# Performance work log

Hardware: AMD Instinct MI355X
Metric: run time of the kernel (lower is better)

The kernel has to match this reference:

```python
import jax, jax.numpy as jnp
import numpy as np

L, M, B = 32768, 8, 8192      # lines, max neighbors per line, blocks
LIN, BIN, H = 768, 768, 512   # line_in_dim, block_in_dim, hidden_size
NH, DH = 8, 512 // 8          # heads, head_dim
LN_EPS = 1e-5


def _ln(x, g, b):
    mu = jnp.mean(x, axis=-1, keepdims=True)
    var = jnp.mean(jnp.square(x - mu), axis=-1, keepdims=True)
    return (x - mu) * jax.lax.rsqrt(var + LN_EPS) * g + b


def setup_inputs() -> dict:
    key = jax.random.key(0)
    ks = jax.random.split(key, 12)
    w = lambda k, shape, fan: jax.random.normal(k, shape, jnp.float32) * (fan ** -0.5)
    return {
        'global_lines': jax.random.normal(ks[0], (L, LIN), jnp.float32),
        'block_reprs': jax.random.normal(ks[1], (B, BIN), jnp.float32),
        'Wq': w(ks[2], (H, LIN), LIN),            # q_proj (no bias)
        'Wkv': w(ks[3], (H, BIN), BIN),           # kv_proj (no bias)
        'qn_g': jnp.ones((H,), jnp.float32), 'qn_b': jnp.zeros((H,), jnp.float32),
        'kvn_g': jnp.ones((H,), jnp.float32), 'kvn_b': jnp.zeros((H,), jnp.float32),
        'in_proj_w': w(ks[4], (3 * H, H), H), 'in_proj_b': jnp.zeros((3 * H,), jnp.float32),
        'out_w': w(ks[5], (H, H), H), 'out_b': jnp.zeros((H,), jnp.float32),
        'p1_w': w(ks[6], (H, 2 * H), 2 * H), 'p1_b': jnp.zeros((H,), jnp.float32),
        'ln1_g': jnp.ones((H,), jnp.float32), 'ln1_b': jnp.zeros((H,), jnp.float32),
        'p2_w': w(ks[7], (H, H), H), 'p2_b': jnp.zeros((H,), jnp.float32),
        'ln2_g': jnp.ones((H,), jnp.float32), 'ln2_b': jnp.zeros((H,), jnp.float32),
        'head_w': w(ks[8], (1, H), H), 'head_b': jnp.zeros((1,), jnp.float32),
        'K_indices': jax.random.randint(ks[9], (L, M), 0, B, jnp.int32),
        'neighbor_counts': jnp.clip(jax.random.randint(ks[10], (L,), 0, M + 1, jnp.int32), 1, M),
    }


def reference(global_lines, block_reprs, Wq, Wkv, qn_g, qn_b, kvn_g, kvn_b,
              in_proj_w, in_proj_b, out_w, out_b,
              p1_w, p1_b, ln1_g, ln1_b, p2_w, p2_b, ln2_g, ln2_b,
              head_w, head_b, K_indices, neighbor_counts):
    # q = LN(q_proj(lines))                              [L, H]
    q = _ln(global_lines @ Wq.T, qn_g, qn_b)
    # gather neighbor block reprs, project, LN           [L, M, H]
    kv = _ln(block_reprs[K_indices] @ Wkv.T, kvn_g, kvn_b)
    pad = jnp.arange(M)[None, :] >= neighbor_counts[:, None]  # True = padded key

    # torch nn.MultiheadAttention with query length 1 per line
    wq_i, wk_i, wv_i = jnp.split(in_proj_w, 3, axis=0)
    bq_i, bk_i, bv_i = jnp.split(in_proj_b, 3, axis=0)
    qh = (q @ wq_i.T + bq_i).reshape(L, NH, DH)
    kh = (kv @ wk_i.T + bk_i).reshape(L, M, NH, DH)
    vh = (kv @ wv_i.T + bv_i).reshape(L, M, NH, DH)
    scores = jnp.einsum('lhd,lmhd->lhm', qh, kh) / np.float32(np.sqrt(DH))
    scores = jnp.where(pad[:, None, :], jnp.finfo(scores.dtype).min, scores)
    attn = jax.nn.softmax(scores, axis=-1)
    ctx = jnp.einsum('lhm,lmhd->lhd', attn, vh).reshape(L, H)
    attn_out = ctx @ out_w.T + out_b

    # line_proj: Linear(2H->H) + LN + GELU + residual(Linear + LN + GELU)
    x = jnp.concatenate([q, attn_out], axis=-1)
    x = jax.nn.gelu(_ln(x @ p1_w.T + p1_b, ln1_g, ln1_b), approximate=False)
    x = x + jax.nn.gelu(_ln(x @ p2_w.T + p2_b, ln2_g, ln2_b), approximate=False)
    logits = (x @ head_w.T + head_b)[:, 0]
    return jax.nn.sigmoid(logits)
```

## Files before the change

kernel.cpp:

```cpp
#include <hip/hip_runtime.h>
#include <math.h>


typedef unsigned short u16;
typedef unsigned int u32;
using bf16x8 = __attribute__((ext_vector_type(8))) __bf16;
using u16x8  = __attribute__((ext_vector_type(8))) u16;
using f32x4  = __attribute__((ext_vector_type(4))) float;

__device__ __forceinline__ u16 f2bf(float f) {
    u32 u = __builtin_bit_cast(u32, f);
    u32 r = u + 0x7fffu + ((u >> 16) & 1u);
    return (u16)(r >> 16);
}
__device__ __forceinline__ float bf2f(u16 h) {
    return __builtin_bit_cast(float, (u32)h << 16);
}
__device__ __forceinline__ float gelu_exact(float x) {
    return 0.5f * x * (1.0f + erff(x * 0.70710678118654752440f));
}

__device__ __forceinline__ float breduce1(float s0, float* sm) {
    #pragma unroll
    for (int off = 32; off > 0; off >>= 1) s0 += __shfl_down(s0, off);
    const int lane = threadIdx.x & 63, w = threadIdx.x >> 6;
    __syncthreads();
    if (lane == 0) sm[w] = s0;
    __syncthreads();
    return sm[0] + sm[1] + sm[2] + sm[3];
}

struct CvtJobs {
    const float* s[5];
    u16* d[5];
    int cum[6];
};
__global__ __launch_bounds__(256) void cvt_multi(CvtJobs j)
{
    const int g = blockIdx.x * 256 + threadIdx.x;
    if (g >= j.cum[5]) return;
    int seg = 0;
    #pragma unroll
    for (int k = 1; k < 5; ++k) seg += (g >= j.cum[k]);
    const int q = g - j.cum[seg];
    const float4 v = *reinterpret_cast<const float4*>(j.s[seg] + q * 4);
    ushort4 o = make_ushort4(f2bf(v.x), f2bf(v.y), f2bf(v.z), f2bf(v.w));
    *reinterpret_cast<ushort4*>(j.d[seg] + q * 4) = o;
}

__global__ __launch_bounds__(256) void fold_w2(
    const float* __restrict__ p1w, const float* __restrict__ outw,
    u16* __restrict__ p1cb)
{
    __shared__ float As[16][65];
    __shared__ float Bs[16][65];
    const int tx = threadIdx.x & 15, ty = threadIdx.x >> 4;
    const int i0 = blockIdx.y * 64, j0 = blockIdx.x * 64;
    const int lr = threadIdx.x >> 2;
    const int lc = (threadIdx.x & 3) * 4;
    const int kr = threadIdx.x >> 4;
    const int jc = (threadIdx.x & 15) * 4;
    float acc[4][4] = {};
    for (int k0 = 0; k0 < 512; k0 += 16) {
        const float4 av = *reinterpret_cast<const float4*>(
            p1w + (size_t)(i0 + lr) * 1024 + 512 + k0 + lc);
        As[lc + 0][lr] = av.x; As[lc + 1][lr] = av.y;
        As[lc + 2][lr] = av.z; As[lc + 3][lr] = av.w;
        const float4 bv = *reinterpret_cast<const float4*>(
            outw + (size_t)(k0 + kr) * 512 + j0 + jc);
        Bs[kr][jc + 0] = bv.x; Bs[kr][jc + 1] = bv.y;
        Bs[kr][jc + 2] = bv.z; Bs[kr][jc + 3] = bv.w;
        __syncthreads();
        #pragma unroll
        for (int kk = 0; kk < 16; ++kk) {
            float a[4], b[4];
            #pragma unroll
            for (int i = 0; i < 4; ++i) a[i] = As[kk][ty * 4 + i];
            #pragma unroll
            for (int jj = 0; jj < 4; ++jj) b[jj] = Bs[kk][tx * 4 + jj];
            #pragma unroll
            for (int i = 0; i < 4; ++i)
                #pragma unroll
                for (int jj = 0; jj < 4; ++jj)
                    acc[i][jj] = fmaf(a[i], b[jj], acc[i][jj]);
        }
        __syncthreads();
    }
    #pragma unroll
    for (int i = 0; i < 4; ++i)
        #pragma unroll
        for (int jj = 0; jj < 4; ++jj)
            p1cb[(size_t)(i0 + ty * 4 + i) * 1024 + 512 + j0 + tx * 4 + jj] =
                f2bf(acc[i][jj]);
}

__global__ __launch_bounds__(64) void fold_bias(
    const float* __restrict__ p1w, const float* __restrict__ outb,
    const float* __restrict__ p1b, float* __restrict__ bias2)
{
    const int i = blockIdx.x, lane = threadIdx.x;
    float s = 0.0f;
    #pragma unroll
    for (int k = lane; k < 512; k += 64)
        s += p1w[(size_t)i * 1024 + 512 + k] * outb[k];
    #pragma unroll
    for (int off = 32; off > 0; off >>= 1) s += __shfl_down(s, off);
    if (lane == 0) bias2[i] = s + p1b[i];
}

template<int A_MODE, bool STATS>
__global__ __launch_bounds__(256) void gemm_bf16(
    const void* __restrict__ A1v, const void* __restrict__ A2v, int K1, int K,
    const u16* __restrict__ W, const float* __restrict__ bias,
    u16* __restrict__ C, int N, float* __restrict__ stats)
{
    __shared__ __bf16 As[2 * 64 * 32];
    __shared__ __bf16 Ws[2 * 128 * 32];
    const int tid = threadIdx.x;
    const int w = tid >> 6, lane = tid & 63;

    const u32 nx = gridDim.x;
    const u32 orig = blockIdx.y * nx + blockIdx.x;
    const u32 nwg = nx * gridDim.y;
    const u32 wgid = (orig & 7u) * (nwg >> 3) + (orig >> 3);
    const int bx = wgid % nx;
    const int row0 = (int)(wgid / nx) * 64;
    const int col0 = bx * 128;

    const int wrow = (w >> 1) * 32, wcol = (w & 1) * 64;
    const int fr = lane & 15, fg = lane >> 4;

    int srow[2], scol[2], soff[2];
    #pragma unroll
    for (int c = 0; c < 2; ++c) {
        const int bo = w * 2048 + c * 1024 + lane * 16;
        srow[c] = bo >> 6;
        scol[c] = (bo & 63) >> 1;
        soff[c] = (w * 2048 + c * 1024) >> 1;
    }
    const int aoA = w * 1024 + lane * 16;
    const int srA = aoA >> 6;
    const int scA = (aoA & 63) >> 1;
    const int sofA = (w * 1024) >> 1;
    const int ar = tid >> 2;
    const int ac = (tid & 3) * 8;

    f32x4 acc[2][4] = {};
    float4 av0, av1;

    auto stage_issue = [&](int k0, int buf) {
        if (A_MODE == 1) {
            const float* src = (const float*)A1v + (size_t)(row0 + ar) * K + k0 + ac;
            av0 = *reinterpret_cast<const float4*>(src);
            av1 = *reinterpret_cast<const float4*>(src + 4);
        } else {
            const u16* asrc;
            if (A_MODE == 2) {
                const bool first = (k0 < K1);
                const u16* base = first ? (const u16*)A1v : (const u16*)A2v;
                const int ldk = first ? K1 : (K - K1);
                const int kk  = first ? k0 : (k0 - K1);
                asrc = base + (size_t)(row0 + srA) * ldk + kk + scA;
            } else {
                asrc = (const u16*)A1v + (size_t)(row0 + srA) * K + k0 + scA;
            }
            __builtin_amdgcn_global_load_lds(
                (const __attribute__((address_space(1))) u32*)asrc,
                (__attribute__((address_space(3))) u32*)(As + buf * 2048 + sofA),
                16, 0, 0);
        }
        #pragma unroll
        for (int c = 0; c < 2; ++c) {
            const u16* wsrc = W + (size_t)(col0 + srow[c]) * K + k0 + scol[c];
            __builtin_amdgcn_global_load_lds(
                (const __attribute__((address_space(1))) u32*)wsrc,
                (__attribute__((address_space(3))) u32*)(Ws + buf * 4096 + soff[c]),
                16, 0, 0);
        }
    };
    auto stage_write = [&](int buf) {
        u16x8 o0;
        o0[0] = f2bf(av0.x); o0[1] = f2bf(av0.y); o0[2] = f2bf(av0.z); o0[3] = f2bf(av0.w);
        o0[4] = f2bf(av1.x); o0[5] = f2bf(av1.y); o0[6] = f2bf(av1.z); o0[7] = f2bf(av1.w);
        *reinterpret_cast<u16x8*>((u16*)As + buf * 2048 + ar * 32 + ac) = o0;
    };

    const int NT = K >> 5;
    int cur = 0;

    stage_issue(0, 0);
    if (A_MODE == 1) stage_write(0);
    __syncthreads();

    for (int t = 0; t < NT; ++t) {
        const bool hn = (t + 1 < NT);
        if (hn) stage_issue((t + 1) << 5, cur ^ 1);

        bf16x8 af[2], bfr[4];
        #pragma unroll
        for (int m = 0; m < 2; ++m)
            af[m] = *(const bf16x8*)(As + cur * 2048 + (wrow + m * 16 + fr) * 32 + fg * 8);
        #pragma unroll
        for (int n = 0; n < 4; ++n)
            bfr[n] = *(const bf16x8*)(Ws + cur * 4096 + (wcol + n * 16 + fr) * 32 + fg * 8);
        #pragma unroll
        for (int m = 0; m < 2; ++m)
            #pragma unroll
            for (int n = 0; n < 4; ++n)
                acc[m][n] = __builtin_amdgcn_mfma_f32_16x16x32_bf16(
                    af[m], bfr[n], acc[m][n], 0, 0, 0);

        if (hn && A_MODE == 1) stage_write(cur ^ 1);
        __syncthreads();
        cur ^= 1;
    }

    if (bias) {
        #pragma unroll
        for (int n = 0; n < 4; ++n) {
            const float bvv = bias[col0 + wcol + n * 16 + fr];
            #pragma unroll
            for (int m = 0; m < 2; ++m)
                #pragma unroll
                for (int r = 0; r < 4; ++r)
                    acc[m][n][r] += bvv;
        }
    }

    #pragma unroll
    for (int m = 0; m < 2; ++m)
        #pragma unroll
        for (int n = 0; n < 4; ++n) {
            const int col = col0 + wcol + n * 16 + fr;
            #pragma unroll
            for (int r = 0; r < 4; ++r) {
                const int row = row0 + wrow + m * 16 + fg * 4 + r;
                C[(size_t)row * N + col] = f2bf(acc[m][n][r]);
            }
        }

    if (STATS) {
        float ps[2][4], pq[2][4];
        #pragma unroll
        for (int m = 0; m < 2; ++m)
            #pragma unroll
            for (int r = 0; r < 4; ++r) {
                float s = 0.0f, q2 = 0.0f;
                #pragma unroll
                for (int n = 0; n < 4; ++n) {
                    const float v = acc[m][n][r];
                    s += v; q2 = fmaf(v, v, q2);
                }
                ps[m][r] = s; pq[m][r] = q2;
            }
        #pragma unroll
        for (int off = 1; off < 16; off <<= 1)
            #pragma unroll
            for (int m = 0; m < 2; ++m)
                #pragma unroll
                for (int r = 0; r < 4; ++r) {
                    ps[m][r] += __shfl_xor(ps[m][r], off);
                    pq[m][r] += __shfl_xor(pq[m][r], off);
                }
        if (fr == 0) {
            const int cb = bx * 2 + (w & 1);
            #pragma unroll
            for (int m = 0; m < 2; ++m)
                #pragma unroll
                for (int r = 0; r < 4; ++r) {
                    const int row = row0 + wrow + m * 16 + fg * 4 + r;
                    *reinterpret_cast<float2*>(stats + ((size_t)row * 8 + cb) * 2) =
                        make_float2(ps[m][r], pq[m][r]);
                }
        }
    }
}

template<bool GELU>
__global__ __launch_bounds__(256) void ln_rows_s(
    u16* __restrict__ X, const float* __restrict__ stats,
    const float* __restrict__ g, const float* __restrict__ b)
{
    const size_t row = blockIdx.x;
    float s = 0.0f, q2 = 0.0f;
    #pragma unroll
    for (int cb = 0; cb < 8; ++cb) {
        s  += stats[(row * 8 + cb) * 2];
        q2 += stats[(row * 8 + cb) * 2 + 1];
    }
    const float mu = s * (1.0f / 512.0f);
    const float var = q2 * (1.0f / 512.0f) - mu * mu;
    const float rs = rsqrtf(var + 1e-5f);
    const int t = threadIdx.x;
    const ushort2 xv = *reinterpret_cast<const ushort2*>(X + row * 512 + 2 * t);
    const float2 gg = *reinterpret_cast<const float2*>(g + 2 * t);
    const float2 bb = *reinterpret_cast<const float2*>(b + 2 * t);
    float y0 = (bf2f(xv.x) - mu) * rs * gg.x + bb.x;
    float y1 = (bf2f(xv.y) - mu) * rs * gg.y + bb.y;
    if (GELU) { y0 = gelu_exact(y0); y1 = gelu_exact(y1); }
    *reinterpret_cast<ushort2*>(X + row * 512 + 2 * t) = make_ushort2(f2bf(y0), f2bf(y1));
}

__global__ __launch_bounds__(512) void attn_kernel(
    const u16* __restrict__ qh, const u16* __restrict__ kvb,
    const int* __restrict__ kidx, const int* __restrict__ ncnt,
    u16* __restrict__ ctx)
{
    const int head = threadIdx.x >> 6;
    const int lane = threadIdx.x & 63;
    const int mi = lane & 7, dg = lane >> 3;
    const bool b0 = (mi & 1), b1 = (mi & 2), b2 = (mi & 4);
    const int doff = (b0 ? 4 : 0) + (b1 ? 2 : 0) + (b2 ? 1 : 0);

    for (int l = blockIdx.x; l < 32768; l += gridDim.x) {
        const int cnt = ncnt[l];
        const int idx = kidx[l * 8 + mi];
        const size_t kvbase = (size_t)idx * 1024 + head * 64 + dg * 8;

        const u16x8 qv = *(const u16x8*)(qh + (size_t)l * 512 + head * 64 + dg * 8);
        const u16x8 kv = *(const u16x8*)(kvb + kvbase);
        const u16x8 vv = *(const u16x8*)(kvb + kvbase + 512);

        float p = 0.0f;
        #pragma unroll
        for (int jj = 0; jj < 8; ++jj) p = fmaf(bf2f(qv[jj]), bf2f(kv[jj]), p);
        p += __shfl_xor(p, 8); p += __shfl_xor(p, 16); p += __shfl_xor(p, 32);

        float s = (mi < cnt) ? p * 0.125f : -3.402823466e38f;
        float mx = s;
        mx = fmaxf(mx, __shfl_xor(mx, 1));
        mx = fmaxf(mx, __shfl_xor(mx, 2));
        mx = fmaxf(mx, __shfl_xor(mx, 4));
        const float e = __expf(s - mx);
        float den = e;
        den += __shfl_xor(den, 1); den += __shfl_xor(den, 2); den += __shfl_xor(den, 4);
        const float wgt = e / den;

        float c[8];
        #pragma unroll
        for (int jj = 0; jj < 8; ++jj) c[jj] = wgt * bf2f(vv[jj]);

        #pragma unroll
        for (int jj = 0; jj < 4; ++jj) {
            const float snd = b0 ? c[jj] : c[jj + 4];
            const float rec = __shfl_xor(snd, 1);
            c[jj] = (b0 ? c[jj + 4] : c[jj]) + rec;
        }
        #pragma unroll
        for (int jj = 0; jj < 2; ++jj) {
            const float snd = b1 ? c[jj] : c[jj + 2];
            const float rec = __shfl_xor(snd, 2);
            c[jj] = (b1 ? c[jj + 2] : c[jj]) + rec;
        }
        {
            const float snd = b2 ? c[0] : c[1];
            const float rec = __shfl_xor(snd, 4);
            c[0] = (b2 ? c[1] : c[0]) + rec;
        }
        ctx[(size_t)l * 512 + head * 64 + dg * 8 + doff] = f2bf(c[0]);
    }
}

__global__ __launch_bounds__(256) void final_head_s(
    const u16* __restrict__ h1, const u16* __restrict__ h2raw,
    const float* __restrict__ stats,
    const float* __restrict__ g, const float* __restrict__ b,
    const float* __restrict__ hw, const float* __restrict__ hb,
    float* __restrict__ out)
{
    __shared__ float sm[4];
    const size_t row = blockIdx.x;
    float s = 0.0f, q2 = 0.0f;
    #pragma unroll
    for (int cb = 0; cb < 8; ++cb) {
        s  += stats[(row * 8 + cb) * 2];
        q2 += stats[(row * 8 + cb) * 2 + 1];
    }
    const float mu = s * (1.0f / 512.0f);
    const float var = q2 * (1.0f / 512.0f) - mu * mu;
    const float rs = rsqrtf(var + 1e-5f);
    const int t = threadIdx.x;
    const ushort2 xv = *reinterpret_cast<const ushort2*>(h2raw + row * 512 + 2 * t);
    const ushort2 hv = *reinterpret_cast<const ushort2*>(h1 + row * 512 + 2 * t);
    const float2 gg = *reinterpret_cast<const float2*>(g + 2 * t);
    const float2 bb = *reinterpret_cast<const float2*>(b + 2 * t);
    const float2 hwv = *reinterpret_cast<const float2*>(hw + 2 * t);
    const float y0 = bf2f(hv.x) + gelu_exact((bf2f(xv.x) - mu) * rs * gg.x + bb.x);
    const float y1 = bf2f(hv.y) + gelu_exact((bf2f(xv.y) - mu) * rs * gg.y + bb.y);
    const float d = breduce1(y0 * hwv.x + y1 * hwv.y, sm);
    if (t == 0) out[row] = 1.0f / (1.0f + expf(-(d + hb[0])));
}

extern "C" void kernel_launch(void* const* d_in, const int* in_sizes, int n_in,
                              void* d_out, int out_size, void* d_ws, size_t ws_size,
                              hipStream_t stream)
{
    const float* lines  = (const float*)d_in[0];
    const float* blocks = (const float*)d_in[1];
    const float* Wq     = (const float*)d_in[2];
    const float* Wkv    = (const float*)d_in[3];
    const float* qn_g   = (const float*)d_in[4];
    const float* qn_b   = (const float*)d_in[5];
    const float* kvn_g  = (const float*)d_in[6];
    const float* kvn_b  = (const float*)d_in[7];
    const float* in_w   = (const float*)d_in[8];
    const float* in_b   = (const float*)d_in[9];
    const float* out_w  = (const float*)d_in[10];
    const float* out_b  = (const float*)d_in[11];
    const float* p1_w   = (const float*)d_in[12];
    const float* p1_b   = (const float*)d_in[13];
    const float* ln1_g  = (const float*)d_in[14];
    const float* ln1_b  = (const float*)d_in[15];
    const float* p2_w   = (const float*)d_in[16];
    const float* p2_b   = (const float*)d_in[17];
    const float* ln2_g  = (const float*)d_in[18];
    const float* ln2_b  = (const float*)d_in[19];
    const float* head_w = (const float*)d_in[20];
    const float* head_b = (const float*)d_in[21];
    const int*   kidx   = (const int*)d_in[22];
    const int*   ncnt   = (const int*)d_in[23];
    float* out = (float*)d_out;

    char* wsb = (char*)d_ws;
    u16* qb    = (u16*)(wsb);
    u16* qhb   = (u16*)(wsb + (32ull << 20));
    u16* ctxb  = (u16*)(wsb + (64ull << 20));
    u16* kvbb  = (u16*)(wsb + (96ull << 20));
    u16* bkvb  = (u16*)(wsb + (112ull << 20));
    float* stats_q   = (float*)(wsb + (120ull << 20));
    float* stats_h1  = (float*)(wsb + (124ull << 20));
    float* stats_h2  = (float*)(wsb + (128ull << 20));
    float* stats_bkv = (float*)(wsb + (132ull << 20));
    u16* Wqb   = (u16*)(wsb + (136ull << 20));
    u16* Wkvb  = Wqb + 512 * 768;
    u16* inwb  = Wkvb + 512 * 768;
    u16* p1cb  = inwb + 1536 * 512;
    u16* p2wb  = p1cb + 512 * 1024;
    float* bias2f = (float*)(p2wb + 512 * 512);

    {
        CvtJobs j;
        const float* ss[5] = { Wq, Wkv, in_w, p1_w, p2_w };
        u16* dd[5] = { Wqb, Wkvb, inwb, p1cb, p2wb };
        const int nn[5] = { 512 * 768, 512 * 768, 1536 * 512, 512 * 1024, 512 * 512 };
        int c = 0;
        for (int k = 0; k < 5; ++k) { j.s[k] = ss[k]; j.d[k] = dd[k]; j.cum[k] = c; c += nn[k] / 4; }
        j.cum[5] = c;
        cvt_multi<<<(c + 255) / 256, 256, 0, stream>>>(j);
    }
    fold_w2<<<dim3(8, 8), 256, 0, stream>>>(p1_w, out_w, p1cb);
    fold_bias<<<512, 64, 0, stream>>>(p1_w, out_b, p1_b, bias2f);

    gemm_bf16<1, true><<<dim3(4, 128), 256, 0, stream>>>(
        blocks, nullptr, 768, 768, Wkvb, nullptr, bkvb, 512, stats_bkv);
    ln_rows_s<false><<<8192, 256, 0, stream>>>(bkvb, stats_bkv, kvn_g, kvn_b);
    gemm_bf16<0, false><<<dim3(8, 128), 256, 0, stream>>>(
        bkvb, nullptr, 512, 512, inwb + 512 * 512, in_b + 512, kvbb, 1024, nullptr);
    gemm_bf16<1, true><<<dim3(4, 512), 256, 0, stream>>>(
        lines, nullptr, 768, 768, Wqb, nullptr, qb, 512, stats_q);
    ln_rows_s<false><<<32768, 256, 0, stream>>>(qb, stats_q, qn_g, qn_b);
    gemm_bf16<0, false><<<dim3(4, 512), 256, 0, stream>>>(
        qb, nullptr, 512, 512, inwb, in_b, qhb, 512, nullptr);
    attn_kernel<<<2048, 512, 0, stream>>>(qhb, kvbb, kidx, ncnt, ctxb);
    gemm_bf16<2, true><<<dim3(4, 512), 256, 0, stream>>>(
        qb, ctxb, 512, 1024, p1cb, bias2f, qhb, 512, stats_h1);
    ln_rows_s<true><<<32768, 256, 0, stream>>>(qhb, stats_h1, ln1_g, ln1_b);
    gemm_bf16<0, true><<<dim3(4, 512), 256, 0, stream>>>(
        qhb, nullptr, 512, 512, p2wb, p2_b, ctxb, 512, stats_h2);
    final_head_s<<<32768, 256, 0, stream>>>(qhb, ctxb, stats_h2, ln2_g, ln2_b,
                                            head_w, head_b, out);
}
```

Measured before the change: 429.2 us.

## Pre-convert fp32 inputs to bf16 and triple-buffer GEMM LDS loads

Adds standalone kernels that convert the fp32 line and block inputs to bf16 in workspace. Every GEMM can then stage A through asynchronous global-to-LDS loads instead of a register fp32-to-bf16 path, which removes the special A_MODE 1 branch. The GEMM main loop moves from double to triple buffering, keeping two stages in flight with explicit vmcnt waits and raw barriers. The cost is an extra full read and write pass over the large input matrices, plus more LDS per block, which may lower occupancy.

```diff
diff --git a/kernel.cpp b/kernel.cpp
--- a/kernel.cpp
+++ b/kernel.cpp
@@ -28,6 +28,16 @@
     if (lane == 0) sm[w] = s0;
     __syncthreads();
     return sm[0] + sm[1] + sm[2] + sm[3];
+}
+
+__global__ __launch_bounds__(256) void cvt_bf16(
+    const float* __restrict__ s, u16* __restrict__ d, int n)
+{
+    const int i = (blockIdx.x * 256 + threadIdx.x) * 4;
+    if (i >= n) return;
+    const float4 v = *reinterpret_cast<const float4*>(s + i);
+    ushort4 o = make_ushort4(f2bf(v.x), f2bf(v.y), f2bf(v.z), f2bf(v.w));
+    *reinterpret_cast<ushort4*>(d + i) = o;
 }
 
 struct CvtJobs {
@@ -110,12 +120,12 @@
 
 template<int A_MODE, bool STATS>
 __global__ __launch_bounds__(256) void gemm_bf16(
-    const void* __restrict__ A1v, const void* __restrict__ A2v, int K1, int K,
+    const u16* __restrict__ A1, const u16* __restrict__ A2, int K1, int K,
     const u16* __restrict__ W, const float* __restrict__ bias,
     u16* __restrict__ C, int N, float* __restrict__ stats)
 {
-    __shared__ __bf16 As[2 * 64 * 32];
-    __shared__ __bf16 Ws[2 * 128 * 32];
+    __shared__ __bf16 As[3 * 64 * 32];
+    __shared__ __bf16 Ws[3 * 128 * 32];
     const int tid = threadIdx.x;
     const int w = tid >> 6, lane = tid & 63;
 
@@ -142,33 +152,21 @@
     const int srA = aoA >> 6;
     const int scA = (aoA & 63) >> 1;
     const int sofA = (w * 1024) >> 1;
-    const int ar = tid >> 2;
-    const int ac = (tid & 3) * 8;
 
     f32x4 acc[2][4] = {};
-    float4 av0, av1;
 
     auto stage_issue = [&](int k0, int buf) {
-        if (A_MODE == 1) {
-            const float* src = (const float*)A1v + (size_t)(row0 + ar) * K + k0 + ac;
-            av0 = *reinterpret_cast<const float4*>(src);
-            av1 = *reinterpret_cast<const float4*>(src + 4);
+        const u16* asrc;
+        if (A_MODE == 2 && k0 >= K1) {
+            asrc = A2 + (size_t)(row0 + srA) * (K - K1) + (k0 - K1) + scA;
         } else {
-            const u16* asrc;
-            if (A_MODE == 2) {
-                const bool first = (k0 < K1);
-                const u16* base = first ? (const u16*)A1v : (const u16*)A2v;
-                const int ldk = first ? K1 : (K - K1);
-                const int kk  = first ? k0 : (k0 - K1);
-                asrc = base + (size_t)(row0 + srA) * ldk + kk + scA;
-            } else {
-                asrc = (const u16*)A1v + (size_t)(row0 + srA) * K + k0 + scA;
-            }
-            __builtin_amdgcn_global_load_lds(
-                (const __attribute__((address_space(1))) u32*)asrc,
-                (__attribute__((address_space(3))) u32*)(As + buf * 2048 + sofA),
-                16, 0, 0);
-        }
+            const int ld = (A_MODE == 2) ? K1 : K;
+            asrc = A1 + (size_t)(row0 + srA) * ld + k0 + scA;
+        }
+        __builtin_amdgcn_global_load_lds(
+            (const __attribute__((address_space(1))) u32*)asrc,
+            (__attribute__((address_space(3))) u32*)(As + buf * 2048 + sofA),
+            16, 0, 0);
         #pragma unroll
         for (int c = 0; c < 2; ++c) {
             const u16* wsrc = W + (size_t)(col0 + srow[c]) * K + k0 + scol[c];
@@ -178,31 +176,34 @@
                 16, 0, 0);
         }
     };
-    auto stage_write = [&](int buf) {
-        u16x8 o0;
-        o0[0] = f2bf(av0.x); o0[1] = f2bf(av0.y); o0[2] = f2bf(av0.z); o0[3] = f2bf(av0.w);
-        o0[4] = f2bf(av1.x); o0[5] = f2bf(av1.y); o0[6] = f2bf(av1.z); o0[7] = f2bf(av1.w);
-        *reinterpret_cast<u16x8*>((u16*)As + buf * 2048 + ar * 32 + ac) = o0;
-    };
 
     const int NT = K >> 5;
-    int cur = 0;
 
     stage_issue(0, 0);
-    if (A_MODE == 1) stage_write(0);
-    __syncthreads();
-
+    stage_issue(32, 1);
+
+    int bufc = 0;
     for (int t = 0; t < NT; ++t) {
-        const bool hn = (t + 1 < NT);
-        if (hn) stage_issue((t + 1) << 5, cur ^ 1);
+        const int ahead = NT - 1 - t;
+        if (ahead >= 2) {
+            int b2 = bufc + 2; if (b2 >= 3) b2 -= 3;
+            stage_issue((t + 2) << 5, b2);
+            asm volatile("s_waitcnt vmcnt(6)" ::: "memory");
+        } else if (ahead == 1) {
+            asm volatile("s_waitcnt vmcnt(3)" ::: "memory");
+        } else {
+            asm volatile("s_waitcnt vmcnt(0)" ::: "memory");
+        }
+        __builtin_amdgcn_s_barrier();
+        __builtin_amdgcn_sched_barrier(0);
 
         bf16x8 af[2], bfr[4];
         #pragma unroll
         for (int m = 0; m < 2; ++m)
-            af[m] = *(const bf16x8*)(As + cur * 2048 + (wrow + m * 16 + fr) * 32 + fg * 8);
+            af[m] = *(const bf16x8*)(As + bufc * 2048 + (wrow + m * 16 + fr) * 32 + fg * 8);
         #pragma unroll
         for (int n = 0; n < 4; ++n)
-            bfr[n] = *(const bf16x8*)(Ws + cur * 4096 + (wcol + n * 16 + fr) * 32 + fg * 8);
+            bfr[n] = *(const bf16x8*)(Ws + bufc * 4096 + (wcol + n * 16 + fr) * 32 + fg * 8);
         #pragma unroll
         for (int m = 0; m < 2; ++m)
             #pragma unroll
@@ -210,9 +211,8 @@
                 acc[m][n] = __builtin_amdgcn_mfma_f32_16x16x32_bf16(
                     af[m], bfr[n], acc[m][n], 0, 0, 0);
 
-        if (hn && A_MODE == 1) stage_write(cur ^ 1);
-        __syncthreads();
-        cur ^= 1;
+        __builtin_amdgcn_s_barrier();
+        bufc = bufc + 1; if (bufc >= 3) bufc -= 3;
     }
 
     if (bias) {
@@ -424,7 +424,9 @@
     char* wsb = (char*)d_ws;
     u16* qb    = (u16*)(wsb);
     u16* qhb   = (u16*)(wsb + (32ull << 20));
+    u16* Lb    = (u16*)(wsb + (32ull << 20));
     u16* ctxb  = (u16*)(wsb + (64ull << 20));
+    u16* Bb    = (u16*)(wsb + (80ull << 20));
     u16* kvbb  = (u16*)(wsb + (96ull << 20));
     u16* bkvb  = (u16*)(wsb + (112ull << 20));
     float* stats_q   = (float*)(wsb + (120ull << 20));
@@ -438,6 +440,8 @@
     u16* p2wb  = p1cb + 512 * 1024;
     float* bias2f = (float*)(p2wb + 512 * 512);
 
+    cvt_bf16<<<(32768 * 768 / 4 + 255) / 256, 256, 0, stream>>>(lines, Lb, 32768 * 768);
+    cvt_bf16<<<(8192 * 768 / 4 + 255) / 256, 256, 0, stream>>>(blocks, Bb, 8192 * 768);
     {
         CvtJobs j;
         const float* ss[5] = { Wq, Wkv, in_w, p1_w, p2_w };
@@ -451,13 +455,13 @@
     fold_w2<<<dim3(8, 8), 256, 0, stream>>>(p1_w, out_w, p1cb);
     fold_bias<<<512, 64, 0, stream>>>(p1_w, out_b, p1_b, bias2f);
 
-    gemm_bf16<1, true><<<dim3(4, 128), 256, 0, stream>>>(
-        blocks, nullptr, 768, 768, Wkvb, nullptr, bkvb, 512, stats_bkv);
+    gemm_bf16<0, true><<<dim3(4, 128), 256, 0, stream>>>(
+        Bb, nullptr, 768, 768, Wkvb, nullptr, bkvb, 512, stats_bkv);
     ln_rows_s<false><<<8192, 256, 0, stream>>>(bkvb, stats_bkv, kvn_g, kvn_b);
     gemm_bf16<0, false><<<dim3(8, 128), 256, 0, stream>>>(
         bkvb, nullptr, 512, 512, inwb + 512 * 512, in_b + 512, kvbb, 1024, nullptr);
-    gemm_bf16<1, true><<<dim3(4, 512), 256, 0, stream>>>(
-        lines, nullptr, 768, 768, Wqb, nullptr, qb, 512, stats_q);
+    gemm_bf16<0, true><<<dim3(4, 512), 256, 0, stream>>>(
+        Lb, nullptr, 768, 768, Wqb, nullptr, qb, 512, stats_q);
     ln_rows_s<false><<<32768, 256, 0, stream>>>(qb, stats_q, qn_g, qn_b);
     gemm_bf16<0, false><<<dim3(4, 512), 256, 0, stream>>>(
         qb, nullptr, 512, 512, inwb, in_b, qhb, 512, nullptr);
```

Measured after the change: 437.1 us. No clear change (+1.8%).
